# Kernel optimization log

Hardware: AMD Instinct MI355X
Metric: run time of the kernel (lower is better)

Reference implementation:

```python
import jax, jax.numpy as jnp
import numpy as np

NODE_DIM = 128
CAT = 16
N_NODES = 100000
N_EDGES = 200000
N_SCALARS = 6
INPUT_DIM = 5 * NODE_DIM + 5 * CAT + N_SCALARS  # 726
CELL_H, NET_H, OUT = 192, 128, 128
EPS = 1e-5


def setup_inputs() -> dict:
    key = jax.random.key(0)
    ks = jax.random.split(key, 24)
    inp = {
        'h_nodes': jax.random.normal(ks[0], (N_NODES, NODE_DIM), jnp.float32),
        'edge_scalars': jax.random.normal(ks[1], (N_EDGES, N_SCALARS), jnp.float32),
        'edge_src': jax.random.randint(ks[2], (N_EDGES,), 0, N_NODES),
        'edge_dst': jax.random.randint(ks[3], (N_EDGES,), 0, N_NODES),
        'edge_type': jax.random.randint(ks[4], (N_EDGES,), 0, 2),
        'cell_type_src': jax.random.randint(ks[5], (N_EDGES,), 0, 256),
        'cell_type_dst': jax.random.randint(ks[6], (N_EDGES,), 0, 256),
        'pin_role_src': jax.random.randint(ks[7], (N_EDGES,), 0, 64),
        'pin_role_dst': jax.random.randint(ks[8], (N_EDGES,), 0, 64),
        # embedding tables
        'emb_edge_type': jax.random.normal(ks[9], (2, CAT), jnp.float32),
        'emb_cell_type': jax.random.normal(ks[10], (256, CAT), jnp.float32),
        'emb_pin_role': jax.random.normal(ks[11], (64, CAT), jnp.float32),
        # cell MLP params
        'cell_W1': jax.random.normal(ks[12], (INPUT_DIM, CELL_H), jnp.float32) * (1.0 / np.sqrt(INPUT_DIM)),
        'cell_b1': jnp.zeros((CELL_H,), jnp.float32),
        'cell_g': jnp.ones((CELL_H,), jnp.float32),
        'cell_beta': jnp.zeros((CELL_H,), jnp.float32),
        'cell_W2': jax.random.normal(ks[13], (CELL_H, OUT), jnp.float32) * (1.0 / np.sqrt(CELL_H)),
        'cell_b2': jnp.zeros((OUT,), jnp.float32),
        # net MLP params
        'net_W1': jax.random.normal(ks[14], (INPUT_DIM, NET_H), jnp.float32) * (1.0 / np.sqrt(INPUT_DIM)),
        'net_b1': jnp.zeros((NET_H,), jnp.float32),
        'net_g': jnp.ones((NET_H,), jnp.float32),
        'net_beta': jnp.zeros((NET_H,), jnp.float32),
        'net_W2': jax.random.normal(ks[15], (NET_H, OUT), jnp.float32) * (1.0 / np.sqrt(NET_H)),
        'net_b2': jnp.zeros((OUT,), jnp.float32),
    }
    return inp


def _oov(x, n):
    return jnp.where((x >= 0) & (x < n), x, 0)


def _mlp(x, W1, b1, g, beta, W2, b2):
    h = x @ W1 + b1
    mu = jnp.mean(h, axis=-1, keepdims=True)
    var = jnp.mean(jnp.square(h - mu), axis=-1, keepdims=True)
    h = (h - mu) * jax.lax.rsqrt(var + EPS) * g + beta
    h = jax.nn.relu(h)
    return h @ W2 + b2


def reference(h_nodes, edge_scalars, emb_edge_type, emb_cell_type, emb_pin_role,
              cell_W1, cell_b1, cell_g, cell_beta, cell_W2, cell_b2,
              net_W1, net_b1, net_g, net_beta, net_W2, net_b2,
              edge_src, edge_dst, edge_type, cell_type_src, cell_type_dst,
              pin_role_src, pin_role_dst):
    h_u = h_nodes[edge_src]                      # [E, D]
    h_v = h_nodes[edge_dst]
    h_prod = h_u * h_v
    h_abs_diff = jnp.abs(h_u - h_v)
    h_signed_diff = h_v - h_u
    e_et = emb_edge_type[_oov(edge_type, emb_edge_type.shape[0])]
    e_ct_s = emb_cell_type[_oov(cell_type_src, emb_cell_type.shape[0])]
    e_ct_d = emb_cell_type[_oov(cell_type_dst, emb_cell_type.shape[0])]
    e_pr_s = emb_pin_role[_oov(pin_role_src, emb_pin_role.shape[0])]
    e_pr_d = emb_pin_role[_oov(pin_role_dst, emb_pin_role.shape[0])]
    scal = jnp.clip(edge_scalars, -10.0, 10.0)
    feat = jnp.concatenate([h_u, h_v, h_prod, h_abs_diff, h_signed_diff,
                            e_et, e_ct_s, e_ct_d, e_pr_s, e_pr_d, scal], axis=-1)  # [E, 726]
    out_cell = _mlp(feat, cell_W1, cell_b1, cell_g, cell_beta, cell_W2, cell_b2)
    out_net = _mlp(feat, net_W1, net_b1, net_g, net_beta, net_W2, net_b2)
    et = edge_type[:, None]
    h_edges = jnp.where(et == 0, out_cell, jnp.where(et == 1, out_net, jnp.zeros_like(out_cell)))
    return h_edges
```

## Files before the change

### kernel.cpp

```cpp
#include <hip/hip_runtime.h>

#define KS   23
#define FPAD 744
#define BM   32

typedef short bfrag8 __attribute__((ext_vector_type(8)));
typedef float f32x4 __attribute__((ext_vector_type(4)));

__device__ __forceinline__ unsigned short f2bf(float f) {
  union { float f; unsigned u; } v; v.f = f;
  unsigned r = v.u + 0x7fffu + ((v.u >> 16) & 1u);
  return (unsigned short)(r >> 16);
}
__device__ __forceinline__ unsigned pk2(float a, float b) {
  return (unsigned)f2bf(a) | ((unsigned)f2bf(b) << 16);
}

__global__ void prep_weights(const float* __restrict__ cW1, const float* __restrict__ nW1,
                             const float* __restrict__ cW2, const float* __restrict__ nW2,
                             unsigned short* __restrict__ w1c, unsigned short* __restrict__ w1n,
                             unsigned short* __restrict__ w2c, unsigned short* __restrict__ w2n,
                             int* __restrict__ cnt) {
  int i = blockIdx.x * blockDim.x + threadIdx.x;
  if (i == 0) { cnt[0] = 0; cnt[1] = 0; }
  const int T0 = 12 * KS * 512, T1 = 8 * KS * 512, T2 = 8 * 6 * 512, T3 = 8 * 4 * 512;
  const int tot = T0 + T1 + T2 + T3;
  for (; i < tot; i += gridDim.x * blockDim.x) {
    int idx = i;
    const float* src; unsigned short* dst; int N, Kreal, KSm, rel;
    if (idx < T0)              { src = cW1; dst = w1c; N = 192; Kreal = 726; KSm = KS; rel = idx; }
    else if ((idx -= T0) < T1) { src = nW1; dst = w1n; N = 128; Kreal = 726; KSm = KS; rel = idx; }
    else if ((idx -= T1) < T2) { src = cW2; dst = w2c; N = 128; Kreal = 192; KSm = 6;  rel = idx; }
    else { idx -= T2;            src = nW2; dst = w2n; N = 128; Kreal = 128; KSm = 4;  rel = idx; }
    int blk = rel >> 9, within = rel & 511;
    int l = within >> 3, e = within & 7;
    int n16 = blk / KSm, k32 = blk - n16 * KSm;
    int n = n16 * 16 + (l & 15);
    int k = k32 * 32 + ((l >> 4) * 8) + e;
    dst[rel] = f2bf(k < Kreal ? src[(size_t)k * N + n] : 0.f);
  }
}

__global__ void compact_edges(const int* __restrict__ et,
                              const int* __restrict__ esrc, const int* __restrict__ edst,
                              const int* __restrict__ cts, const int* __restrict__ ctd,
                              const int* __restrict__ prs, const int* __restrict__ prd,
                              int* __restrict__ cnt, int4* __restrict__ r0, int4* __restrict__ r1,
                              float* __restrict__ out, int n) {
  int i = blockIdx.x * blockDim.x + threadIdx.x;
  for (; i < n; i += gridDim.x * blockDim.x) {
    int ty = et[i];
    if (ty == 0 || ty == 1) {
      int c1 = cts[i]; c1 = ((unsigned)c1 < 256u) ? c1 : 0;
      int c2 = ctd[i]; c2 = ((unsigned)c2 < 256u) ? c2 : 0;
      int p1 = prs[i]; p1 = ((unsigned)p1 < 64u)  ? p1 : 0;
      int p2 = prd[i]; p2 = ((unsigned)p2 < 64u)  ? p2 : 0;
      int4 rec; rec.x = esrc[i]; rec.y = edst[i]; rec.z = i;
      rec.w = c1 | (c2 << 8) | (p1 << 16) | (p2 << 22);
      if (ty == 0) r0[atomicAdd(&cnt[0], 1)] = rec;
      else         r1[atomicAdd(&cnt[1], 1)] = rec;
    } else {
      float4 z = make_float4(0.f, 0.f, 0.f, 0.f);
      float4* po = (float4*)(out + (size_t)i * 128);
      #pragma unroll
      for (int j = 0; j < 32; ++j) po[j] = z;
    }
  }
}

template <int CH>
__device__ __forceinline__ void mlp_tile(
    char* smraw, int* sEid, int tile, int c, int etv,
    const int4* __restrict__ rec,
    const float* __restrict__ h_nodes, const float* __restrict__ edge_scalars,
    const float* __restrict__ emb_et, const float* __restrict__ emb_ct, const float* __restrict__ emb_pr,
    const unsigned short* __restrict__ w1f, const unsigned short* __restrict__ w2f,
    const float* __restrict__ b1, const float* __restrict__ g,
    const float* __restrict__ beta, const float* __restrict__ b2,
    float* __restrict__ out)
{
  constexpr int NF  = CH / 64;
  constexpr int KS2 = CH / 32;
  constexpr int CHP = CH + 8;
  unsigned short (*feat)[FPAD] = (unsigned short (*)[FPAD])smraw;
  unsigned short (*hb)[CHP]    = (unsigned short (*)[CHP])smraw;
  float (*red)[BM][2] = (float (*)[BM][2])(smraw + BM * CHP * 2);
  float (*murs)[2]    = (float (*)[2])(smraw + BM * CHP * 2 + 4 * BM * 2 * 4);

  const int t    = threadIdx.x;
  const int lane = t & 63;
  const int wid  = t >> 6;
  const int lrow = lane & 15;
  const int kq   = (lane >> 4) * 8;
  const int base = tile * BM;
  const int r    = t >> 3;
  const int l8   = t & 7;

  float b1r[NF], gr[NF], ber[NF];
  #pragma unroll
  for (int nf = 0; nf < NF; ++nf) {
    int n = wid * (CH / 4) + nf * 16 + lrow;
    b1r[nf] = b1[n]; gr[nf] = g[n]; ber[nf] = beta[n];
  }
  float b2r[2];
  #pragma unroll
  for (int nf2 = 0; nf2 < 2; ++nf2) b2r[nf2] = b2[wid * 32 + nf2 * 16 + lrow];

  const int idx  = base + r;
  const bool valid = idx < c;
  int4 q = rec[valid ? idx : (c - 1)];
  if (l8 == 0) sEid[r] = valid ? q.z : -1;

  const float* bu = h_nodes + (size_t)q.x * 128;
  const float* bv = h_nodes + (size_t)q.y * 128;
  float4 ub[4], vb[4];
  #pragma unroll
  for (int j = 0; j < 4; ++j) {
    const int d = (l8 + 8 * j) * 4;
    ub[j] = *(const float4*)(bu + d);
    vb[j] = *(const float4*)(bv + d);
  }
  const int pk = q.w;
  const int c1 = pk & 255, c2 = (pk >> 8) & 255, p1 = (pk >> 16) & 63, p2 = (pk >> 22) & 63;
  const float* tp = (l8 == 0) ? emb_et + etv * 16
                  : (l8 == 1) ? emb_ct + c1 * 16
                  : (l8 == 2) ? emb_ct + c2 * 16
                  : (l8 == 3) ? emb_pr + p1 * 16
                  :             emb_pr + p2 * 16;
  float4 e4[4];
  if (l8 < 5) {
    #pragma unroll
    for (int j = 0; j < 4; ++j) e4[j] = ((const float4*)tp)[j];
  }
  float2 sc2[3];
  if (l8 == 5) {
    const float2* sp = (const float2*)(edge_scalars + (size_t)q.z * 6);
    #pragma unroll
    for (int j = 0; j < 3; ++j) sc2[j] = sp[j];
  }

  if (valid) {
    #pragma unroll
    for (int j = 0; j < 4; ++j) {
      const int d = (l8 + 8 * j) * 4;
      float ua[4] = {ub[j].x, ub[j].y, ub[j].z, ub[j].w};
      float va[4] = {vb[j].x, vb[j].y, vb[j].z, vb[j].w};
      uint2 s0 = make_uint2(pk2(ua[0], ua[1]), pk2(ua[2], ua[3]));
      uint2 s1 = make_uint2(pk2(va[0], va[1]), pk2(va[2], va[3]));
      uint2 s2 = make_uint2(pk2(ua[0] * va[0], ua[1] * va[1]), pk2(ua[2] * va[2], ua[3] * va[3]));
      uint2 s3 = make_uint2(pk2(fabsf(ua[0] - va[0]), fabsf(ua[1] - va[1])),
                            pk2(fabsf(ua[2] - va[2]), fabsf(ua[3] - va[3])));
      uint2 s4 = make_uint2(pk2(va[0] - ua[0], va[1] - ua[1]), pk2(va[2] - ua[2], va[3] - ua[3]));
      *(uint2*)&feat[r][0 * 128 + d] = s0;
      *(uint2*)&feat[r][1 * 128 + d] = s1;
      *(uint2*)&feat[r][2 * 128 + d] = s2;
      *(uint2*)&feat[r][3 * 128 + d] = s3;
      *(uint2*)&feat[r][4 * 128 + d] = s4;
    }
  } else {
    uint2 z = make_uint2(0u, 0u);
    #pragma unroll
    for (int j = 0; j < 4; ++j) {
      const int d = (l8 + 8 * j) * 4;
      #pragma unroll
      for (int s = 0; s < 5; ++s) *(uint2*)&feat[r][s * 128 + d] = z;
    }
  }
  if (l8 < 5) {
    float va[16];
    #pragma unroll
    for (int j = 0; j < 4; ++j) {
      va[4 * j + 0] = e4[j].x; va[4 * j + 1] = e4[j].y;
      va[4 * j + 2] = e4[j].z; va[4 * j + 3] = e4[j].w;
    }
    if (!valid) {
      #pragma unroll
      for (int j = 0; j < 16; ++j) va[j] = 0.f;
    }
    uint4 w0 = make_uint4(pk2(va[0], va[1]), pk2(va[2], va[3]), pk2(va[4], va[5]), pk2(va[6], va[7]));
    uint4 w1_ = make_uint4(pk2(va[8], va[9]), pk2(va[10], va[11]), pk2(va[12], va[13]), pk2(va[14], va[15]));
    *(uint4*)&feat[r][640 + l8 * 16 + 0] = w0;
    *(uint4*)&feat[r][640 + l8 * 16 + 8] = w1_;
  } else if (l8 == 5) {
    float sv[6] = {sc2[0].x, sc2[0].y, sc2[1].x, sc2[1].y, sc2[2].x, sc2[2].y};
    #pragma unroll
    for (int j = 0; j < 6; ++j)
      sv[j] = valid ? fminf(fmaxf(sv[j], -10.f), 10.f) : 0.f;
    uint4 w0 = make_uint4(pk2(sv[0], sv[1]), pk2(sv[2], sv[3]), pk2(sv[4], sv[5]), 0u);
    uint4 w1_ = make_uint4(0u, 0u, 0u, 0u);
    *(uint4*)&feat[r][720 + 0] = w0;
    *(uint4*)&feat[r][720 + 8] = w1_;
  }
  __syncthreads();

  f32x4 acc1[2][NF];
  #pragma unroll
  for (int mf = 0; mf < 2; ++mf)
    #pragma unroll
    for (int nf = 0; nf < NF; ++nf) acc1[mf][nf] = 0;
  const unsigned short* wb = w1f + ((size_t)wid * NF * KS) * 512 + (size_t)lane * 8;
  bfrag8 br[3][NF];
  #pragma unroll
  for (int nf = 0; nf < NF; ++nf) {
    br[0][nf] = *(const bfrag8*)(wb + ((size_t)nf * KS + 0) * 512);
    br[1][nf] = *(const bfrag8*)(wb + ((size_t)nf * KS + 1) * 512);
  }
  #pragma unroll
  for (int k = 0; k < KS; ++k) {
    if (k + 2 < KS) {
      #pragma unroll
      for (int nf = 0; nf < NF; ++nf)
        br[(k + 2) % 3][nf] = *(const bfrag8*)(wb + ((size_t)nf * KS + (k + 2)) * 512);
    }
    bfrag8 a0 = *(const bfrag8*)&feat[lrow][k * 32 + kq];
    bfrag8 a1 = *(const bfrag8*)&feat[16 + lrow][k * 32 + kq];
    #pragma unroll
    for (int nf = 0; nf < NF; ++nf) {
      acc1[0][nf] = __builtin_amdgcn_mfma_f32_16x16x32_bf16(a0, br[k % 3][nf], acc1[0][nf], 0, 0, 0);
      acc1[1][nf] = __builtin_amdgcn_mfma_f32_16x16x32_bf16(a1, br[k % 3][nf], acc1[1][nf], 0, 0, 0);
    }
  }

  bfrag8 cr[KS2][2];
  const unsigned short* wb2 = w2f + (size_t)lane * 8;
  #pragma unroll
  for (int k2 = 0; k2 < KS2; ++k2)
    #pragma unroll
    for (int nf2 = 0; nf2 < 2; ++nf2)
      cr[k2][nf2] = *(const bfrag8*)(wb2 + ((size_t)(2 * wid + nf2) * KS2 + k2) * 512);

  __syncthreads();

  float sums[2][4], sqs[2][4];
  #pragma unroll
  for (int mf = 0; mf < 2; ++mf)
    #pragma unroll
    for (int rg = 0; rg < 4; ++rg) {
      float s = 0.f, qd = 0.f;
      #pragma unroll
      for (int nf = 0; nf < NF; ++nf) {
        float v = acc1[mf][nf][rg] + b1r[nf];
        acc1[mf][nf][rg] = v;
        s += v; qd += v * v;
      }
      sums[mf][rg] = s; sqs[mf][rg] = qd;
    }
  #pragma unroll
  for (int d = 1; d < 16; d <<= 1) {
    #pragma unroll
    for (int mf = 0; mf < 2; ++mf)
      #pragma unroll
      for (int rg = 0; rg < 4; ++rg) {
        sums[mf][rg] += __shfl_xor(sums[mf][rg], d);
        sqs[mf][rg]  += __shfl_xor(sqs[mf][rg], d);
      }
  }
  if (lrow == 0) {
    const int qr = lane >> 4;
    #pragma unroll
    for (int mf = 0; mf < 2; ++mf)
      #pragma unroll
      for (int rg = 0; rg < 4; ++rg) {
        int row = mf * 16 + qr * 4 + rg;
        red[wid][row][0] = sums[mf][rg];
        red[wid][row][1] = sqs[mf][rg];
      }
  }
  __syncthreads();
  if (t < BM) {
    float ss = red[0][t][0] + red[1][t][0] + red[2][t][0] + red[3][t][0];
    float qq = red[0][t][1] + red[1][t][1] + red[2][t][1] + red[3][t][1];
    float m = ss * (1.f / CH);
    float va = fmaxf(qq * (1.f / CH) - m * m, 0.f);
    murs[t][0] = m;
    murs[t][1] = rsqrtf(va + 1e-5f);
  }
  __syncthreads();

  #pragma unroll
  for (int mf = 0; mf < 2; ++mf)
    #pragma unroll
    for (int rg = 0; rg < 4; ++rg) {
      int row = mf * 16 + (lane >> 4) * 4 + rg;
      float m = murs[row][0], rv = murs[row][1];
      #pragma unroll
      for (int nf = 0; nf < NF; ++nf) {
        float v = (acc1[mf][nf][rg] - m) * rv * gr[nf] + ber[nf];
        hb[row][wid * (CH / 4) + nf * 16 + lrow] = f2bf(fmaxf(v, 0.f));
      }
    }
  __syncthreads();

  f32x4 acc2[2][2];
  #pragma unroll
  for (int mf = 0; mf < 2; ++mf) { acc2[mf][0] = 0; acc2[mf][1] = 0; }
  #pragma unroll
  for (int k2 = 0; k2 < KS2; ++k2) {
    bfrag8 a0 = *(const bfrag8*)&hb[lrow][k2 * 32 + kq];
    bfrag8 a1 = *(const bfrag8*)&hb[16 + lrow][k2 * 32 + kq];
    #pragma unroll
    for (int nf2 = 0; nf2 < 2; ++nf2) {
      acc2[0][nf2] = __builtin_amdgcn_mfma_f32_16x16x32_bf16(a0, cr[k2][nf2], acc2[0][nf2], 0, 0, 0);
      acc2[1][nf2] = __builtin_amdgcn_mfma_f32_16x16x32_bf16(a1, cr[k2][nf2], acc2[1][nf2], 0, 0, 0);
    }
  }

  #pragma unroll
  for (int mf = 0; mf < 2; ++mf)
    #pragma unroll
    for (int rg = 0; rg < 4; ++rg) {
      int row = mf * 16 + (lane >> 4) * 4 + rg;
      int eid = sEid[row];
      if (eid >= 0) {
        float* po = out + (size_t)eid * 128 + wid * 32 + lrow;
        #pragma unroll
        for (int nf2 = 0; nf2 < 2; ++nf2)
          po[nf2 * 16] = acc2[mf][nf2][rg] + b2r[nf2];
      }
    }
}

struct Args {
  const float *h_nodes, *edge_scalars;
  const float *emb_et, *emb_ct, *emb_pr;
  const unsigned short *w1c, *w2c;
  const float *cb1, *cg, *cbe, *cb2;
  const unsigned short *w1n, *w2n;
  const float *nb1, *ng, *nbe, *nb2;
  const int *cnt;
  const int4 *r0, *r1;
  float* out;
};

__global__ __launch_bounds__(256, 4) void edge_mlp_all(Args A) {
  __shared__ alignas(16) char smraw[BM * FPAD * 2];
  __shared__ int sEid[BM];
  const int c0 = A.cnt[0];
  const int nb0 = (c0 + BM - 1) / BM;
  const int b = blockIdx.x;
  if (b < nb0) {
    mlp_tile<192>(smraw, sEid, b, c0, 0, A.r0, A.h_nodes, A.edge_scalars,
                  A.emb_et, A.emb_ct, A.emb_pr, A.w1c, A.w2c,
                  A.cb1, A.cg, A.cbe, A.cb2, A.out);
  } else {
    const int c1 = A.cnt[1];
    const int t2 = b - nb0;
    if (t2 * BM < c1)
      mlp_tile<128>(smraw, sEid, t2, c1, 1, A.r1, A.h_nodes, A.edge_scalars,
                    A.emb_et, A.emb_ct, A.emb_pr, A.w1n, A.w2n,
                    A.nb1, A.ng, A.nbe, A.nb2, A.out);
  }
}

extern "C" void kernel_launch(void* const* d_in, const int* in_sizes, int n_in,
                              void* d_out, int out_size, void* d_ws, size_t ws_size,
                              hipStream_t stream) {
  (void)n_in; (void)out_size; (void)ws_size;
  const float* h_nodes      = (const float*)d_in[0];
  const float* edge_scalars = (const float*)d_in[1];
  const int*   edge_src     = (const int*)d_in[2];
  const int*   edge_dst     = (const int*)d_in[3];
  const int*   edge_type    = (const int*)d_in[4];
  const int*   ct_s         = (const int*)d_in[5];
  const int*   ct_d         = (const int*)d_in[6];
  const int*   pr_s         = (const int*)d_in[7];
  const int*   pr_d         = (const int*)d_in[8];
  const float* emb_et       = (const float*)d_in[9];
  const float* emb_ct       = (const float*)d_in[10];
  const float* emb_pr       = (const float*)d_in[11];
  const float* cW1 = (const float*)d_in[12];
  const float* cb1 = (const float*)d_in[13];
  const float* cg  = (const float*)d_in[14];
  const float* cbe = (const float*)d_in[15];
  const float* cW2 = (const float*)d_in[16];
  const float* cb2 = (const float*)d_in[17];
  const float* nW1 = (const float*)d_in[18];
  const float* nb1 = (const float*)d_in[19];
  const float* ng  = (const float*)d_in[20];
  const float* nbe = (const float*)d_in[21];
  const float* nW2 = (const float*)d_in[22];
  const float* nb2 = (const float*)d_in[23];
  const int n_edges = in_sizes[2];
  float* out = (float*)d_out;

  char* ws = (char*)d_ws;
  int* cnt = (int*)ws;
  int4* r0 = (int4*)(ws + 256);
  int4* r1 = r0 + n_edges;
  size_t woff = (256 + (size_t)2 * n_edges * sizeof(int4) + 255) & ~(size_t)255;
  unsigned short* w1c = (unsigned short*)(ws + woff);
  unsigned short* w1n = w1c + 12 * KS * 512;
  unsigned short* w2c = w1n + 8 * KS * 512;
  unsigned short* w2n = w2c + 8 * 6 * 512;

  prep_weights<<<1080, 256, 0, stream>>>(cW1, nW1, cW2, nW2, w1c, w1n, w2c, w2n, cnt);
  compact_edges<<<(n_edges + 255) / 256, 256, 0, stream>>>(edge_type, edge_src, edge_dst,
                                                           ct_s, ct_d, pr_s, pr_d,
                                                           cnt, r0, r1, out, n_edges);

  Args A;
  A.h_nodes = h_nodes; A.edge_scalars = edge_scalars;
  A.emb_et = emb_et; A.emb_ct = emb_ct; A.emb_pr = emb_pr;
  A.w1c = w1c; A.w2c = w2c; A.cb1 = cb1; A.cg = cg; A.cbe = cbe; A.cb2 = cb2;
  A.w1n = w1n; A.w2n = w2n; A.nb1 = nb1; A.ng = ng; A.nbe = nbe; A.nb2 = nb2;
  A.cnt = cnt; A.r0 = r0; A.r1 = r1; A.out = out;

  const int nbAll = (n_edges + BM - 1) / BM + 2;
  edge_mlp_all<<<nbAll, 256, 0, stream>>>(A);
}
```

Measured before the change: 213.1 us.

## Stream edge feature tile through double-buffered LDS chunks interleaved with GEMM

Instead of building the full 32x744 bf16 feature tile in LDS before the first GEMM, the kernel now builds it in six column chunks of at most 128 values (h_u, h_v, product, abs diff, signed diff, then embeddings plus scalars). Chunks go into a double-buffered 32x136 LDS area, and each chunk is written while the MFMAs consume the previous one. This shrinks the block's LDS footprint, which may let more blocks share a CU, and overlaps feature construction with matrix work. In exchange it adds a barrier per chunk and drops the triple-buffered register prefetch of W1 fragments, loading them right before use. Invalid rows are no longer zero-filled.

After: 224.6 us. +5.4%, slower.

```diff
diff --git a/kernel.cpp b/kernel.cpp
--- a/kernel.cpp
+++ b/kernel.cpp
@@ -1,8 +1,8 @@
 #include <hip/hip_runtime.h>
 
 #define KS   23
-#define FPAD 744
 #define BM   32
+#define CHK  136
 
 typedef short bfrag8 __attribute__((ext_vector_type(8)));
 typedef float f32x4 __attribute__((ext_vector_type(4)));
@@ -82,10 +82,10 @@
   constexpr int NF  = CH / 64;
   constexpr int KS2 = CH / 32;
   constexpr int CHP = CH + 8;
-  unsigned short (*feat)[FPAD] = (unsigned short (*)[FPAD])smraw;
-  unsigned short (*hb)[CHP]    = (unsigned short (*)[CHP])smraw;
-  float (*red)[BM][2] = (float (*)[BM][2])(smraw + BM * CHP * 2);
-  float (*murs)[2]    = (float (*)[2])(smraw + BM * CHP * 2 + 4 * BM * 2 * 4);
+  unsigned short (*ch)[BM][CHK] = (unsigned short (*)[BM][CHK])smraw;
+  unsigned short (*hb)[CHP]     = (unsigned short (*)[CHP])(smraw + 17408);
+  float (*red)[BM][2] = (float (*)[BM][2])(smraw + 17408 + 12800);
+  float (*murs)[2]    = (float (*)[2])(smraw + 17408 + 12800 + 1024);
 
   const int t    = threadIdx.x;
   const int lane = t & 63;
@@ -139,59 +139,47 @@
     for (int j = 0; j < 3; ++j) sc2[j] = sp[j];
   }
 
-  if (valid) {
-    #pragma unroll
-    for (int j = 0; j < 4; ++j) {
-      const int d = (l8 + 8 * j) * 4;
-      float ua[4] = {ub[j].x, ub[j].y, ub[j].z, ub[j].w};
-      float va[4] = {vb[j].x, vb[j].y, vb[j].z, vb[j].w};
-      uint2 s0 = make_uint2(pk2(ua[0], ua[1]), pk2(ua[2], ua[3]));
-      uint2 s1 = make_uint2(pk2(va[0], va[1]), pk2(va[2], va[3]));
-      uint2 s2 = make_uint2(pk2(ua[0] * va[0], ua[1] * va[1]), pk2(ua[2] * va[2], ua[3] * va[3]));
-      uint2 s3 = make_uint2(pk2(fabsf(ua[0] - va[0]), fabsf(ua[1] - va[1])),
-                            pk2(fabsf(ua[2] - va[2]), fabsf(ua[3] - va[3])));
-      uint2 s4 = make_uint2(pk2(va[0] - ua[0], va[1] - ua[1]), pk2(va[2] - ua[2], va[3] - ua[3]));
-      *(uint2*)&feat[r][0 * 128 + d] = s0;
-      *(uint2*)&feat[r][1 * 128 + d] = s1;
-      *(uint2*)&feat[r][2 * 128 + d] = s2;
-      *(uint2*)&feat[r][3 * 128 + d] = s3;
-      *(uint2*)&feat[r][4 * 128 + d] = s4;
-    }
-  } else {
-    uint2 z = make_uint2(0u, 0u);
-    #pragma unroll
-    for (int j = 0; j < 4; ++j) {
-      const int d = (l8 + 8 * j) * 4;
-      #pragma unroll
-      for (int s = 0; s < 5; ++s) *(uint2*)&feat[r][s * 128 + d] = z;
-    }
-  }
-  if (l8 < 5) {
-    float va[16];
-    #pragma unroll
-    for (int j = 0; j < 4; ++j) {
-      va[4 * j + 0] = e4[j].x; va[4 * j + 1] = e4[j].y;
-      va[4 * j + 2] = e4[j].z; va[4 * j + 3] = e4[j].w;
-    }
-    if (!valid) {
-      #pragma unroll
-      for (int j = 0; j < 16; ++j) va[j] = 0.f;
-    }
-    uint4 w0 = make_uint4(pk2(va[0], va[1]), pk2(va[2], va[3]), pk2(va[4], va[5]), pk2(va[6], va[7]));
-    uint4 w1_ = make_uint4(pk2(va[8], va[9]), pk2(va[10], va[11]), pk2(va[12], va[13]), pk2(va[14], va[15]));
-    *(uint4*)&feat[r][640 + l8 * 16 + 0] = w0;
-    *(uint4*)&feat[r][640 + l8 * 16 + 8] = w1_;
-  } else if (l8 == 5) {
-    float sv[6] = {sc2[0].x, sc2[0].y, sc2[1].x, sc2[1].y, sc2[2].x, sc2[2].y};
-    #pragma unroll
-    for (int j = 0; j < 6; ++j)
-      sv[j] = valid ? fminf(fmaxf(sv[j], -10.f), 10.f) : 0.f;
-    uint4 w0 = make_uint4(pk2(sv[0], sv[1]), pk2(sv[2], sv[3]), pk2(sv[4], sv[5]), 0u);
-    uint4 w1_ = make_uint4(0u, 0u, 0u, 0u);
-    *(uint4*)&feat[r][720 + 0] = w0;
-    *(uint4*)&feat[r][720 + 8] = w1_;
-  }
-  __syncthreads();
+  auto writeChunk = [&](int cc) {
+    unsigned short (*buf)[CHK] = ch[cc & 1];
+    if (cc < 5) {
+      #pragma unroll
+      for (int j = 0; j < 4; ++j) {
+        const int d = (l8 + 8 * j) * 4;
+        float ua[4] = {ub[j].x, ub[j].y, ub[j].z, ub[j].w};
+        float va[4] = {vb[j].x, vb[j].y, vb[j].z, vb[j].w};
+        float x[4];
+        #pragma unroll
+        for (int e = 0; e < 4; ++e) {
+          x[e] = (cc == 0) ? ua[e]
+               : (cc == 1) ? va[e]
+               : (cc == 2) ? ua[e] * va[e]
+               : (cc == 3) ? fabsf(ua[e] - va[e])
+               :             va[e] - ua[e];
+        }
+        *(uint2*)&buf[r][d] = make_uint2(pk2(x[0], x[1]), pk2(x[2], x[3]));
+      }
+    } else {
+      if (l8 < 5) {
+        float va[16];
+        #pragma unroll
+        for (int j = 0; j < 4; ++j) {
+          va[4 * j + 0] = e4[j].x; va[4 * j + 1] = e4[j].y;
+          va[4 * j + 2] = e4[j].z; va[4 * j + 3] = e4[j].w;
+        }
+        uint4 w0 = make_uint4(pk2(va[0], va[1]), pk2(va[2], va[3]), pk2(va[4], va[5]), pk2(va[6], va[7]));
+        uint4 w1_ = make_uint4(pk2(va[8], va[9]), pk2(va[10], va[11]), pk2(va[12], va[13]), pk2(va[14], va[15]));
+        *(uint4*)&buf[r][l8 * 16 + 0] = w0;
+        *(uint4*)&buf[r][l8 * 16 + 8] = w1_;
+      } else if (l8 == 5) {
+        float sv[6] = {sc2[0].x, sc2[0].y, sc2[1].x, sc2[1].y, sc2[2].x, sc2[2].y};
+        #pragma unroll
+        for (int j = 0; j < 6; ++j) sv[j] = fminf(fmaxf(sv[j], -10.f), 10.f);
+        uint4 w0 = make_uint4(pk2(sv[0], sv[1]), pk2(sv[2], sv[3]), pk2(sv[4], sv[5]), 0u);
+        *(uint4*)&buf[r][80] = w0;
+        *(uint4*)&buf[r][88] = make_uint4(0u, 0u, 0u, 0u);
+      }
+    }
+  };
 
   f32x4 acc1[2][NF];
   #pragma unroll
@@ -199,26 +187,28 @@
     #pragma unroll
     for (int nf = 0; nf < NF; ++nf) acc1[mf][nf] = 0;
   const unsigned short* wb = w1f + ((size_t)wid * NF * KS) * 512 + (size_t)lane * 8;
-  bfrag8 br[3][NF];
-  #pragma unroll
-  for (int nf = 0; nf < NF; ++nf) {
-    br[0][nf] = *(const bfrag8*)(wb + ((size_t)nf * KS + 0) * 512);
-    br[1][nf] = *(const bfrag8*)(wb + ((size_t)nf * KS + 1) * 512);
-  }
-  #pragma unroll
-  for (int k = 0; k < KS; ++k) {
-    if (k + 2 < KS) {
-      #pragma unroll
-      for (int nf = 0; nf < NF; ++nf)
-        br[(k + 2) % 3][nf] = *(const bfrag8*)(wb + ((size_t)nf * KS + (k + 2)) * 512);
-    }
-    bfrag8 a0 = *(const bfrag8*)&feat[lrow][k * 32 + kq];
-    bfrag8 a1 = *(const bfrag8*)&feat[16 + lrow][k * 32 + kq];
-    #pragma unroll
-    for (int nf = 0; nf < NF; ++nf) {
-      acc1[0][nf] = __builtin_amdgcn_mfma_f32_16x16x32_bf16(a0, br[k % 3][nf], acc1[0][nf], 0, 0, 0);
-      acc1[1][nf] = __builtin_amdgcn_mfma_f32_16x16x32_bf16(a1, br[k % 3][nf], acc1[1][nf], 0, 0, 0);
-    }
+
+  writeChunk(0);
+  __syncthreads();
+  #pragma unroll
+  for (int cc = 0; cc < 6; ++cc) {
+    if (cc < 5) writeChunk(cc + 1);
+    const int ks = (cc < 5) ? 4 : 3;
+    unsigned short (*buf)[CHK] = ch[cc & 1];
+    #pragma unroll
+    for (int k = 0; k < 4; ++k) {
+      if (k >= ks) break;
+      const int kk = cc * 4 + k;
+      bfrag8 a0 = *(const bfrag8*)&buf[lrow][k * 32 + kq];
+      bfrag8 a1 = *(const bfrag8*)&buf[16 + lrow][k * 32 + kq];
+      #pragma unroll
+      for (int nf = 0; nf < NF; ++nf) {
+        bfrag8 bf = *(const bfrag8*)(wb + ((size_t)nf * KS + kk) * 512);
+        acc1[0][nf] = __builtin_amdgcn_mfma_f32_16x16x32_bf16(a0, bf, acc1[0][nf], 0, 0, 0);
+        acc1[1][nf] = __builtin_amdgcn_mfma_f32_16x16x32_bf16(a1, bf, acc1[1][nf], 0, 0, 0);
+      }
+    }
+    __syncthreads();
   }
 
   bfrag8 cr[KS2][2];
@@ -228,8 +218,6 @@
     #pragma unroll
     for (int nf2 = 0; nf2 < 2; ++nf2)
       cr[k2][nf2] = *(const bfrag8*)(wb2 + ((size_t)(2 * wid + nf2) * KS2 + k2) * 512);
-
-  __syncthreads();
 
   float sums[2][4], sqs[2][4];
   #pragma unroll
@@ -333,7 +321,7 @@
 };
 
 __global__ __launch_bounds__(256, 4) void edge_mlp_all(Args A) {
-  __shared__ alignas(16) char smraw[BM * FPAD * 2];
+  __shared__ alignas(16) char smraw[17408 + 12800 + 1024 + 256];
   __shared__ int sEid[BM];
   const int c0 = A.cnt[0];
   const int nb0 = (c0 + BM - 1) / BM;
```

## Stage MLP output through LDS for coalesced stores and use nontemporal memory ops

Applied to the files above, without the earlier changes.

The final output tile is first staged in shared memory, then each thread writes 64 contiguous bytes per edge row with vector stores, replacing scattered 4-byte stores. Gathers of node rows, edge records and scalars, plus the zero-fill and output stores, become nontemporal loads and stores. The bf16 conversion now uses the HIP intrinsic. The change adds two block barriers and gives up cache retention for node rows that many edges reuse.

Result: slower. 310.5 us (+45.7%).

```diff
diff --git a/kernel.cpp b/kernel.cpp
--- a/kernel.cpp
+++ b/kernel.cpp
@@ -1,4 +1,5 @@
 #include <hip/hip_runtime.h>
+#include <hip/hip_bf16.h>
 
 #define KS   23
 #define FPAD 744
@@ -6,11 +7,14 @@
 
 typedef short bfrag8 __attribute__((ext_vector_type(8)));
 typedef float f32x4 __attribute__((ext_vector_type(4)));
+typedef float f4 __attribute__((ext_vector_type(4)));
+typedef float f2v __attribute__((ext_vector_type(2)));
+typedef int   i4 __attribute__((ext_vector_type(4)));
 
 __device__ __forceinline__ unsigned short f2bf(float f) {
-  union { float f; unsigned u; } v; v.f = f;
-  unsigned r = v.u + 0x7fffu + ((v.u >> 16) & 1u);
-  return (unsigned short)(r >> 16);
+  union { __hip_bfloat16 h; unsigned short s; } v;
+  v.h = __float2bfloat16(f);
+  return v.s;
 }
 __device__ __forceinline__ unsigned pk2(float a, float b) {
   return (unsigned)f2bf(a) | ((unsigned)f2bf(b) << 16);
@@ -60,10 +64,10 @@
       if (ty == 0) r0[atomicAdd(&cnt[0], 1)] = rec;
       else         r1[atomicAdd(&cnt[1], 1)] = rec;
     } else {
-      float4 z = make_float4(0.f, 0.f, 0.f, 0.f);
-      float4* po = (float4*)(out + (size_t)i * 128);
-      #pragma unroll
-      for (int j = 0; j < 32; ++j) po[j] = z;
+      f4 z = {0.f, 0.f, 0.f, 0.f};
+      f4* po = (f4*)(out + (size_t)i * 128);
+      #pragma unroll
+      for (int j = 0; j < 32; ++j) __builtin_nontemporal_store(z, po + j);
     }
   }
 }
@@ -86,6 +90,7 @@
   unsigned short (*hb)[CHP]    = (unsigned short (*)[CHP])smraw;
   float (*red)[BM][2] = (float (*)[BM][2])(smraw + BM * CHP * 2);
   float (*murs)[2]    = (float (*)[2])(smraw + BM * CHP * 2 + 4 * BM * 2 * 4);
+  float (*ot)[132]    = (float (*)[132])smraw;
 
   const int t    = threadIdx.x;
   const int lane = t & 63;
@@ -108,17 +113,17 @@
 
   const int idx  = base + r;
   const bool valid = idx < c;
-  int4 q = rec[valid ? idx : (c - 1)];
+  i4 q = __builtin_nontemporal_load((const i4*)rec + (valid ? idx : (c - 1)));
   if (l8 == 0) sEid[r] = valid ? q.z : -1;
 
   const float* bu = h_nodes + (size_t)q.x * 128;
   const float* bv = h_nodes + (size_t)q.y * 128;
-  float4 ub[4], vb[4];
+  f4 ub[4], vb[4];
   #pragma unroll
   for (int j = 0; j < 4; ++j) {
     const int d = (l8 + 8 * j) * 4;
-    ub[j] = *(const float4*)(bu + d);
-    vb[j] = *(const float4*)(bv + d);
+    ub[j] = __builtin_nontemporal_load((const f4*)(bu + d));
+    vb[j] = __builtin_nontemporal_load((const f4*)(bv + d));
   }
   const int pk = q.w;
   const int c1 = pk & 255, c2 = (pk >> 8) & 255, p1 = (pk >> 16) & 63, p2 = (pk >> 22) & 63;
@@ -132,11 +137,11 @@
     #pragma unroll
     for (int j = 0; j < 4; ++j) e4[j] = ((const float4*)tp)[j];
   }
-  float2 sc2[3];
+  f2v sc2[3];
   if (l8 == 5) {
-    const float2* sp = (const float2*)(edge_scalars + (size_t)q.z * 6);
-    #pragma unroll
-    for (int j = 0; j < 3; ++j) sc2[j] = sp[j];
+    const f2v* sp = (const f2v*)(edge_scalars + (size_t)q.z * 6);
+    #pragma unroll
+    for (int j = 0; j < 3; ++j) sc2[j] = __builtin_nontemporal_load(sp + j);
   }
 
   if (valid) {
@@ -304,20 +309,30 @@
       acc2[1][nf2] = __builtin_amdgcn_mfma_f32_16x16x32_bf16(a1, cr[k2][nf2], acc2[1][nf2], 0, 0, 0);
     }
   }
-
-  #pragma unroll
-  for (int mf = 0; mf < 2; ++mf)
-    #pragma unroll
-    for (int rg = 0; rg < 4; ++rg) {
-      int row = mf * 16 + (lane >> 4) * 4 + rg;
-      int eid = sEid[row];
-      if (eid >= 0) {
-        float* po = out + (size_t)eid * 128 + wid * 32 + lrow;
-        #pragma unroll
-        for (int nf2 = 0; nf2 < 2; ++nf2)
-          po[nf2 * 16] = acc2[mf][nf2][rg] + b2r[nf2];
-      }
-    }
+  __syncthreads();
+
+  #pragma unroll
+  for (int nf2 = 0; nf2 < 2; ++nf2) {
+    int n = wid * 32 + nf2 * 16 + lrow;
+    float bb = b2r[nf2];
+    #pragma unroll
+    for (int mf = 0; mf < 2; ++mf)
+      #pragma unroll
+      for (int rg = 0; rg < 4; ++rg)
+        ot[mf * 16 + (lane >> 4) * 4 + rg][n] = acc2[mf][nf2][rg] + bb;
+  }
+  __syncthreads();
+
+  {
+    const int d0 = l8 * 16;
+    int eid = sEid[r];
+    if (eid >= 0) {
+      f4* po = (f4*)(out + (size_t)eid * 128 + d0);
+      const f4* ps = (const f4*)&ot[r][d0];
+      #pragma unroll
+      for (int j = 0; j < 4; ++j) __builtin_nontemporal_store(ps[j], po + j);
+    }
+  }
 }
 
 struct Args {
```
